# Kernel optimization log

Hardware: AMD Instinct MI355X
Metric: run time of the kernel (lower is better)

The kernel has to match this reference:

```python
import jax, jax.numpy as jnp
import numpy as np

B, T, C, HS = 512, 256, 384, 64

def setup_inputs() -> dict:
    key = jax.random.key(0)
    kx, kq, kk, kv = jax.random.split(key, 4)
    x = jax.random.normal(kx, (B, T, C), dtype=jnp.float32)
    Wq = jax.random.normal(kq, (C, HS), dtype=jnp.float32) * (C ** -0.5)
    Wk = jax.random.normal(kk, (C, HS), dtype=jnp.float32) * (C ** -0.5)
    Wv = jax.random.normal(kv, (C, HS), dtype=jnp.float32) * (C ** -0.5)
    return {"x": x, "Wq": Wq, "Wk": Wk, "Wv": Wv}

def reference(x, Wq, Wk, Wv):
    # single-head causal self-attention (dropout = identity in eval mode)
    q = jnp.einsum('btc,ch->bth', x, Wq)   # [B,T,HS]
    k = jnp.einsum('btc,ch->bth', x, Wk)   # [B,T,HS]
    v = jnp.einsum('btc,ch->bth', x, Wv)   # [B,T,HS]
    scale = k.shape[-1] ** -0.5
    wei = jnp.einsum('bqh,bkh->bqk', q, k) * scale  # [B,T,T]
    causal = jnp.tril(jnp.ones((T, T), dtype=bool))
    wei = jnp.where(causal, wei, -jnp.inf)
    wei = jax.nn.softmax(wei, axis=-1)
    out = jnp.einsum('bqk,bkh->bqh', wei, v)  # [B,T,HS]
    return out
```

## Files before the change

kernel.cpp:

```cpp
#include <hip/hip_runtime.h>


typedef float f32x4 __attribute__((ext_vector_type(4)));
typedef __bf16 bf16x8 __attribute__((ext_vector_type(8)));
typedef short s16x8 __attribute__((ext_vector_type(8)));

constexpr int T_ = 256;
constexpr int C_ = 384;
constexpr int HS_ = 64;
constexpr int QKVE = 512 * 256 * 64;

__device__ __forceinline__ short f2bs(float v) {
  __bf16 b = (__bf16)v;
  return __builtin_bit_cast(short, b);
}

__device__ __forceinline__ f32x4 mfma16(bf16x8 a, bf16x8 b, f32x4 c) {
  return __builtin_amdgcn_mfma_f32_16x16x32_bf16(a, b, c, 0, 0, 0);
}

__device__ __forceinline__ void gl_lds16(const short* g, short* l) {
  __builtin_amdgcn_global_load_lds((const __attribute__((address_space(1))) void*)g,
                                   (__attribute__((address_space(3))) void*)l,
                                   16, 0, 0);
}

__global__ void prep_wt_kernel(const float* __restrict__ Wq,
                               const float* __restrict__ Wk,
                               const float* __restrict__ Wv,
                               short* __restrict__ wt) {
  int idx = blockIdx.x * 256 + threadIdx.x;
  if (idx >= 192 * 384) return;
  int n = idx / 384;
  int k = idx - n * 384;
  const float* W = (n < 64) ? Wq : (n < 128) ? Wk : Wv;
  int h = n & 63;
  wt[idx] = f2bs(W[k * 64 + h]);
}

__global__ __launch_bounds__(256, 3) void qkv_proj(const float* __restrict__ x,
                                                   const short* __restrict__ wt,
                                                   short* __restrict__ ws) {
  __shared__ __align__(16) short wtile[2][4 * 192 * 8];
  __shared__ __align__(16) short vbuf[128][65];

  short* qg = ws;
  short* kg = ws + QKVE;
  short* vtg = ws + 2 * QKVE;

  const int blk = blockIdx.x;
  const int b = blk >> 1;
  const int rowbase = (blk & 1) * 128;
  const int tid = threadIdx.x;
  const int w = tid >> 6;
  const int lane = tid & 63;
  const int lr = tid & 15;
  const int lg = lane >> 4;

  const float* xb = x + (size_t)b * (T_ * C_);

  auto stage = [&](int buf, int ks) {
#pragma unroll
    for (int i = 0; i < 3; ++i) {
      int c = i * 256 + w * 64 + lane;
      int n = c % 192;
      int lgc = c / 192;
      const short* src = wt + n * 384 + ks * 32 + lgc * 8;
      short* dst = &wtile[buf][(i * 256 + w * 64) * 8];
      gl_lds16(src, dst);
    }
  };

  f32x4 xf[2][2], xn[2][2];
  auto loadx = [&](f32x4 dst[2][2], int ks) {
#pragma unroll
    for (int m = 0; m < 2; ++m) {
      int row = rowbase + (2 * w + m) * 16 + lr;
      const f32x4* p = reinterpret_cast<const f32x4*>(xb + (size_t)row * C_ + ks * 32 + lg * 8);
      dst[m][0] = p[0];
      dst[m][1] = p[1];
    }
  };

  f32x4 acc[2][12];
#pragma unroll
  for (int m = 0; m < 2; ++m)
#pragma unroll
    for (int nt = 0; nt < 12; ++nt) acc[m][nt] = f32x4{0.f, 0.f, 0.f, 0.f};

  stage(0, 0);
  loadx(xf, 0);
  __syncthreads();

  for (int ks = 0; ks < 12; ++ks) {
    const int cur = ks & 1;
    if (ks < 11) {
      stage(cur ^ 1, ks + 1);
      loadx(xn, ks + 1);
    }
    bf16x8 a[2];
#pragma unroll
    for (int m = 0; m < 2; ++m) {
      bf16x8 t;
      t[0] = (__bf16)xf[m][0][0]; t[1] = (__bf16)xf[m][0][1];
      t[2] = (__bf16)xf[m][0][2]; t[3] = (__bf16)xf[m][0][3];
      t[4] = (__bf16)xf[m][1][0]; t[5] = (__bf16)xf[m][1][1];
      t[6] = (__bf16)xf[m][1][2]; t[7] = (__bf16)xf[m][1][3];
      a[m] = t;
    }
#pragma unroll
    for (int nt = 0; nt < 12; ++nt) {
      bf16x8 bw = *reinterpret_cast<const bf16x8*>(&wtile[cur][(lg * 192 + nt * 16 + lr) * 8]);
      acc[0][nt] = mfma16(a[0], bw, acc[0][nt]);
      acc[1][nt] = mfma16(a[1], bw, acc[1][nt]);
    }
    __syncthreads();
    if (ks < 11) {
#pragma unroll
      for (int m = 0; m < 2; ++m) {
        xf[m][0] = xn[m][0];
        xf[m][1] = xn[m][1];
      }
    }
  }

  const float QSCALE = 0.125f * 1.44269504f;
#pragma unroll
  for (int nt = 0; nt < 12; ++nt) {
    const int which = nt >> 2;
    const int hb = (nt & 3) * 16 + lr;
#pragma unroll
    for (int m = 0; m < 2; ++m) {
#pragma unroll
      for (int j = 0; j < 4; ++j) {
        int t = rowbase + (2 * w + m) * 16 + lg * 4 + j;
        float v = acc[m][nt][j];
        if (which == 0) {
          qg[(size_t)b * 16384 + t * 64 + hb] = f2bs(v * QSCALE);
        } else if (which == 1) {
          kg[(size_t)b * 16384 + t * 64 + (hb ^ ((t & 7) << 3))] = f2bs(v);
        } else {
          vbuf[t - rowbase][hb] = f2bs(v);
        }
      }
    }
  }
  __syncthreads();

#pragma unroll
  for (int r = 0; r < 4; ++r) {
    int c = r * 256 + tid;
    int h = c >> 4;
    int i = c & 15;
    s16x8 tv;
#pragma unroll
    for (int j = 0; j < 8; ++j) tv[j] = vbuf[i * 8 + j][h];
    int tokbase = (rowbase + i * 8) ^ ((h & 7) << 3);
    *reinterpret_cast<s16x8*>(vtg + (size_t)b * 16384 + h * 256 + tokbase) = tv;
  }
}

__global__ __launch_bounds__(512, 4) void attn(const short* __restrict__ ws,
                                               float* __restrict__ out) {
  __shared__ __align__(16) short KS[256 * 64];
  __shared__ __align__(16) short VT[64 * 256];
  __shared__ __align__(16) short PB[8][16 * 40];

  const short* qg = ws;
  const short* kg = ws + QKVE;
  const short* vtg = ws + 2 * QKVE;

  const int b = blockIdx.x;
  const int tid = threadIdx.x;
  const int w = tid >> 6;
  const int lane = tid & 63;
  const int lr = tid & 15;
  const int lg = lane >> 4;

#pragma unroll
  for (int i = 0; i < 4; ++i) {
    int ch = w * 4 + i;
    gl_lds16(kg + (size_t)b * 16384 + ch * 512 + lane * 8, &KS[ch * 512]);
    gl_lds16(vtg + (size_t)b * 16384 + ch * 512 + lane * 8, &VT[ch * 512]);
  }
  __syncthreads();

  for (int pass = 0; pass < 2; ++pass) {
    const int t = pass ? (15 - w) : w;
    const short* qrow = qg + (size_t)b * 16384 + (t * 16 + lr) * 64;
    bf16x8 aq0 = *reinterpret_cast<const bf16x8*>(qrow + lg * 8);
    bf16x8 aq1 = *reinterpret_cast<const bf16x8*>(qrow + 32 + lg * 8);

    f32x4 o[4];
    float mrun[4], lrun[4];
#pragma unroll
    for (int nt = 0; nt < 4; ++nt) o[nt] = f32x4{0.f, 0.f, 0.f, 0.f};
#pragma unroll
    for (int j = 0; j < 4; ++j) { mrun[j] = -1e30f; lrun[j] = 0.f; }

    const int nkt = (t >> 1) + 1;
    for (int kt = 0; kt < nkt; ++kt) {
      f32x4 s0 = f32x4{0.f, 0.f, 0.f, 0.f};
      f32x4 s1 = f32x4{0.f, 0.f, 0.f, 0.f};
      {
        int kr0 = kt * 32 + lr;
        int kr1 = kr0 + 16;
        bf16x8 b00 = *reinterpret_cast<const bf16x8*>(&KS[kr0 * 64 + ((lg * 8) ^ ((kr0 & 7) << 3))]);
        bf16x8 b01 = *reinterpret_cast<const bf16x8*>(&KS[kr0 * 64 + ((32 + lg * 8) ^ ((kr0 & 7) << 3))]);
        bf16x8 b10 = *reinterpret_cast<const bf16x8*>(&KS[kr1 * 64 + ((lg * 8) ^ ((kr1 & 7) << 3))]);
        bf16x8 b11 = *reinterpret_cast<const bf16x8*>(&KS[kr1 * 64 + ((32 + lg * 8) ^ ((kr1 & 7) << 3))]);
        s0 = mfma16(aq0, b00, s0);
        s0 = mfma16(aq1, b01, s0);
        s1 = mfma16(aq0, b10, s1);
        s1 = mfma16(aq1, b11, s1);
      }

      if (kt == nkt - 1) {
#pragma unroll
        for (int j = 0; j < 4; ++j) {
          int row = t * 16 + lg * 4 + j;
          if (kt * 32 + lr > row)      s0[j] = -1e30f;
          if (kt * 32 + 16 + lr > row) s1[j] = -1e30f;
        }
      }

      float alpha[4];
#pragma unroll
      for (int j = 0; j < 4; ++j) {
        float mx = fmaxf(s0[j], s1[j]);
        mx = fmaxf(mx, __shfl_xor(mx, 1));
        mx = fmaxf(mx, __shfl_xor(mx, 2));
        mx = fmaxf(mx, __shfl_xor(mx, 4));
        mx = fmaxf(mx, __shfl_xor(mx, 8));
        float mnew = fmaxf(mrun[j], mx);
        float al = exp2f(mrun[j] - mnew);
        mrun[j] = mnew;
        alpha[j] = al;
        float e0 = exp2f(s0[j] - mnew);
        float e1 = exp2f(s1[j] - mnew);
        float rs = e0 + e1;
        rs += __shfl_xor(rs, 1);
        rs += __shfl_xor(rs, 2);
        rs += __shfl_xor(rs, 4);
        rs += __shfl_xor(rs, 8);
        lrun[j] = lrun[j] * al + rs;
        int prow = lg * 4 + j;
        PB[w][prow * 40 + lr] = f2bs(e0);
        PB[w][prow * 40 + 16 + lr] = f2bs(e1);
      }

#pragma unroll
      for (int nt = 0; nt < 4; ++nt) {
        o[nt][0] *= alpha[0];
        o[nt][1] *= alpha[1];
        o[nt][2] *= alpha[2];
        o[nt][3] *= alpha[3];
      }
      bf16x8 ap = *reinterpret_cast<const bf16x8*>(&PB[w][lr * 40 + lg * 8]);
#pragma unroll
      for (int nt = 0; nt < 4; ++nt) {
        int h = nt * 16 + lr;
        bf16x8 bv = *reinterpret_cast<const bf16x8*>(&VT[h * 256 + ((kt * 32 + lg * 8) ^ ((h & 7) << 3))]);
        o[nt] = mfma16(ap, bv, o[nt]);
      }
    }

    float inv[4];
#pragma unroll
    for (int j = 0; j < 4; ++j) inv[j] = 1.0f / lrun[j];
    float* ob = out + ((size_t)b * T_ + t * 16 + lg * 4) * HS_;
#pragma unroll
    for (int nt = 0; nt < 4; ++nt)
#pragma unroll
      for (int j = 0; j < 4; ++j)
        ob[j * HS_ + nt * 16 + lr] = o[nt][j] * inv[j];
  }
}

__device__ __forceinline__ int qswz(int row, int h) {
  return row * 64 + (h ^ ((row & 7) << 3));
}
__device__ __forceinline__ int vswz(int h, int tok) {
  return h * 256 + (tok ^ ((h & 7) << 3));
}

__global__ __launch_bounds__(512, 1) void fused_head(const float* __restrict__ x,
                                                     const short* __restrict__ wt,
                                                     float* __restrict__ out) {
  __shared__ __align__(16) short QS[256 * 64];
  __shared__ __align__(16) short KS[256 * 64];
  __shared__ __align__(16) short VT[64 * 256];
  __shared__ __align__(16) short PB[8][16 * 40];

  const int b = blockIdx.x;
  const int tid = threadIdx.x;
  const int w = tid >> 6;
  const int lr = tid & 15;
  const int lg = (tid & 63) >> 4;

  const float* xb = x + (size_t)b * (T_ * C_);

  f32x4 acc[2][12];
#pragma unroll
  for (int m = 0; m < 2; ++m)
#pragma unroll
    for (int nt = 0; nt < 12; ++nt) acc[m][nt] = f32x4{0.f, 0.f, 0.f, 0.f};

#pragma unroll
  for (int ks = 0; ks < 12; ++ks) {
    bf16x8 a[2];
#pragma unroll
    for (int m = 0; m < 2; ++m) {
      int row = (2 * w + m) * 16 + lr;
      const f32x4* p = reinterpret_cast<const f32x4*>(xb + row * C_ + ks * 32 + lg * 8);
      f32x4 f0 = p[0];
      f32x4 f1 = p[1];
      bf16x8 t;
      t[0] = (__bf16)f0[0]; t[1] = (__bf16)f0[1]; t[2] = (__bf16)f0[2]; t[3] = (__bf16)f0[3];
      t[4] = (__bf16)f1[0]; t[5] = (__bf16)f1[1]; t[6] = (__bf16)f1[2]; t[7] = (__bf16)f1[3];
      a[m] = t;
    }
#pragma unroll
    for (int nt = 0; nt < 12; ++nt) {
      bf16x8 bw = *reinterpret_cast<const bf16x8*>(wt + (nt * 16 + lr) * 384 + ks * 32 + lg * 8);
      acc[0][nt] = mfma16(a[0], bw, acc[0][nt]);
      acc[1][nt] = mfma16(a[1], bw, acc[1][nt]);
    }
  }

  const float QSCALE = 0.125f * 1.44269504f;
#pragma unroll
  for (int nt = 0; nt < 12; ++nt) {
    const int which = nt >> 2;
    const int hb = (nt & 3) * 16 + lr;
#pragma unroll
    for (int m = 0; m < 2; ++m) {
      const int rbase = (2 * w + m) * 16 + lg * 4;
#pragma unroll
      for (int j = 0; j < 4; ++j) {
        int row = rbase + j;
        float v = acc[m][nt][j];
        if (which == 0)      QS[qswz(row, hb)] = f2bs(v * QSCALE);
        else if (which == 1) KS[qswz(row, hb)] = f2bs(v);
        else                 VT[vswz(hb, row)] = f2bs(v);
      }
    }
  }

  __syncthreads();

  for (int pass = 0; pass < 2; ++pass) {
    const int t = pass ? (15 - w) : w;
    const int qrow = t * 16 + lr;
    bf16x8 aq0 = *reinterpret_cast<const bf16x8*>(&QS[qswz(qrow, lg * 8)]);
    bf16x8 aq1 = *reinterpret_cast<const bf16x8*>(&QS[qswz(qrow, 32 + lg * 8)]);

    f32x4 o[4];
    float mrun[4], lrun[4];
#pragma unroll
    for (int nt = 0; nt < 4; ++nt) o[nt] = f32x4{0.f, 0.f, 0.f, 0.f};
#pragma unroll
    for (int j = 0; j < 4; ++j) { mrun[j] = -1e30f; lrun[j] = 0.f; }

    const int nkt = (t >> 1) + 1;
    for (int kt = 0; kt < nkt; ++kt) {
      f32x4 s0 = f32x4{0.f, 0.f, 0.f, 0.f};
      f32x4 s1 = f32x4{0.f, 0.f, 0.f, 0.f};
      {
        int kr0 = kt * 32 + lr;
        int kr1 = kr0 + 16;
        bf16x8 b00 = *reinterpret_cast<const bf16x8*>(&KS[qswz(kr0, lg * 8)]);
        bf16x8 b01 = *reinterpret_cast<const bf16x8*>(&KS[qswz(kr0, 32 + lg * 8)]);
        bf16x8 b10 = *reinterpret_cast<const bf16x8*>(&KS[qswz(kr1, lg * 8)]);
        bf16x8 b11 = *reinterpret_cast<const bf16x8*>(&KS[qswz(kr1, 32 + lg * 8)]);
        s0 = mfma16(aq0, b00, s0);
        s0 = mfma16(aq1, b01, s0);
        s1 = mfma16(aq0, b10, s1);
        s1 = mfma16(aq1, b11, s1);
      }

      if (kt == nkt - 1) {
#pragma unroll
        for (int j = 0; j < 4; ++j) {
          int row = t * 16 + lg * 4 + j;
          if (kt * 32 + lr > row)      s0[j] = -1e30f;
          if (kt * 32 + 16 + lr > row) s1[j] = -1e30f;
        }
      }

      float alpha[4];
#pragma unroll
      for (int j = 0; j < 4; ++j) {
        float mx = fmaxf(s0[j], s1[j]);
        mx = fmaxf(mx, __shfl_xor(mx, 1));
        mx = fmaxf(mx, __shfl_xor(mx, 2));
        mx = fmaxf(mx, __shfl_xor(mx, 4));
        mx = fmaxf(mx, __shfl_xor(mx, 8));
        float mnew = fmaxf(mrun[j], mx);
        float al = exp2f(mrun[j] - mnew);
        mrun[j] = mnew;
        alpha[j] = al;
        float e0 = exp2f(s0[j] - mnew);
        float e1 = exp2f(s1[j] - mnew);
        float rs = e0 + e1;
        rs += __shfl_xor(rs, 1);
        rs += __shfl_xor(rs, 2);
        rs += __shfl_xor(rs, 4);
        rs += __shfl_xor(rs, 8);
        lrun[j] = lrun[j] * al + rs;
        int prow = lg * 4 + j;
        PB[w][prow * 40 + lr] = f2bs(e0);
        PB[w][prow * 40 + 16 + lr] = f2bs(e1);
      }

#pragma unroll
      for (int nt = 0; nt < 4; ++nt) {
        o[nt][0] *= alpha[0];
        o[nt][1] *= alpha[1];
        o[nt][2] *= alpha[2];
        o[nt][3] *= alpha[3];
      }
      bf16x8 ap = *reinterpret_cast<const bf16x8*>(&PB[w][lr * 40 + lg * 8]);
#pragma unroll
      for (int nt = 0; nt < 4; ++nt) {
        int h = nt * 16 + lr;
        bf16x8 bv = *reinterpret_cast<const bf16x8*>(&VT[vswz(h, kt * 32 + lg * 8)]);
        o[nt] = mfma16(ap, bv, o[nt]);
      }
    }

    float inv[4];
#pragma unroll
    for (int j = 0; j < 4; ++j) inv[j] = 1.0f / lrun[j];
    float* ob = out + ((size_t)b * T_ + t * 16 + lg * 4) * HS_;
#pragma unroll
    for (int nt = 0; nt < 4; ++nt)
#pragma unroll
      for (int j = 0; j < 4; ++j)
        ob[j * HS_ + nt * 16 + lr] = o[nt][j] * inv[j];
  }
}

extern "C" void kernel_launch(void* const* d_in, const int* in_sizes, int n_in,
                              void* d_out, int out_size, void* d_ws, size_t ws_size,
                              hipStream_t stream) {
  const float* x = (const float*)d_in[0];
  const float* Wq = (const float*)d_in[1];
  const float* Wk = (const float*)d_in[2];
  const float* Wv = (const float*)d_in[3];
  float* out = (float*)d_out;
  short* ws = (short*)d_ws;

  const size_t need = ((size_t)3 * QKVE + 192 * 384) * sizeof(short);

  if (ws_size >= need) {
    short* wt = ws + 3 * QKVE;
    prep_wt_kernel<<<288, 256, 0, stream>>>(Wq, Wk, Wv, wt);
    qkv_proj<<<1024, 256, 0, stream>>>(x, wt, ws);
    attn<<<512, 512, 0, stream>>>(ws, out);
  } else {
    short* wt = ws;
    prep_wt_kernel<<<288, 256, 0, stream>>>(Wq, Wk, Wv, wt);
    fused_head<<<512, 512, 0, stream>>>(x, wt, out);
  }
}
```

Before: 368.1 us.

## Keep full swizzled weight matrix resident in LDS for persistent QKV projection

The QKV projection kernel now loads the whole 192x384 bf16 weight matrix into LDS once per block, using an XOR-swizzled layout written by the prep kernel, so bank conflicts stay low. It then runs 256 blocks of 1024 threads, each wave handling two 16-row tiles with register double-buffered x loads and no per-k-step barriers. The V transpose through LDS is replaced with direct scattered global stores. This is meant to remove repeated weight staging and synchronisation, but it uses about 144KB of LDS per block, limiting occupancy to one block per CU, and the V writes become uncoalesced 2-byte stores.

```diff
diff --git a/kernel.cpp b/kernel.cpp
--- a/kernel.cpp
+++ b/kernel.cpp
@@ -32,131 +32,109 @@
   int idx = blockIdx.x * 256 + threadIdx.x;
   if (idx >= 192 * 384) return;
   int n = idx / 384;
-  int k = idx - n * 384;
+  int kpos = idx - n * 384;
+  int cpos = kpos >> 3;
+  int inner = kpos & 7;
+  int k = ((cpos ^ (n & 7)) << 3) | inner;
   const float* W = (n < 64) ? Wq : (n < 128) ? Wk : Wv;
   int h = n & 63;
   wt[idx] = f2bs(W[k * 64 + h]);
 }
 
-__global__ __launch_bounds__(256, 3) void qkv_proj(const float* __restrict__ x,
-                                                   const short* __restrict__ wt,
-                                                   short* __restrict__ ws) {
-  __shared__ __align__(16) short wtile[2][4 * 192 * 8];
-  __shared__ __align__(16) short vbuf[128][65];
+__global__ __launch_bounds__(1024, 4) void qkv_proj(const float* __restrict__ x,
+                                                    const short* __restrict__ wt,
+                                                    short* __restrict__ ws) {
+  __shared__ __align__(16) short WL[192 * 384];
 
   short* qg = ws;
   short* kg = ws + QKVE;
   short* vtg = ws + 2 * QKVE;
 
-  const int blk = blockIdx.x;
-  const int b = blk >> 1;
-  const int rowbase = (blk & 1) * 128;
   const int tid = threadIdx.x;
   const int w = tid >> 6;
-  const int lane = tid & 63;
   const int lr = tid & 15;
-  const int lg = lane >> 4;
-
-  const float* xb = x + (size_t)b * (T_ * C_);
-
-  auto stage = [&](int buf, int ks) {
-#pragma unroll
-    for (int i = 0; i < 3; ++i) {
-      int c = i * 256 + w * 64 + lane;
-      int n = c % 192;
-      int lgc = c / 192;
-      const short* src = wt + n * 384 + ks * 32 + lgc * 8;
-      short* dst = &wtile[buf][(i * 256 + w * 64) * 8];
-      gl_lds16(src, dst);
-    }
-  };
-
-  f32x4 xf[2][2], xn[2][2];
-  auto loadx = [&](f32x4 dst[2][2], int ks) {
-#pragma unroll
-    for (int m = 0; m < 2; ++m) {
-      int row = rowbase + (2 * w + m) * 16 + lr;
-      const f32x4* p = reinterpret_cast<const f32x4*>(xb + (size_t)row * C_ + ks * 32 + lg * 8);
-      dst[m][0] = p[0];
-      dst[m][1] = p[1];
-    }
-  };
-
-  f32x4 acc[2][12];
-#pragma unroll
-  for (int m = 0; m < 2; ++m)
-#pragma unroll
-    for (int nt = 0; nt < 12; ++nt) acc[m][nt] = f32x4{0.f, 0.f, 0.f, 0.f};
-
-  stage(0, 0);
-  loadx(xf, 0);
+  const int lg = (tid & 63) >> 4;
+
+#pragma unroll
+  for (int i = 0; i < 9; ++i) {
+    gl_lds16(wt + (i * 1024 + tid) * 8, &WL[(i * 1024 + w * 64) * 8]);
+  }
   __syncthreads();
 
-  for (int ks = 0; ks < 12; ++ks) {
-    const int cur = ks & 1;
-    if (ks < 11) {
-      stage(cur ^ 1, ks + 1);
-      loadx(xn, ks + 1);
-    }
-    bf16x8 a[2];
-#pragma unroll
-    for (int m = 0; m < 2; ++m) {
-      bf16x8 t;
-      t[0] = (__bf16)xf[m][0][0]; t[1] = (__bf16)xf[m][0][1];
-      t[2] = (__bf16)xf[m][0][2]; t[3] = (__bf16)xf[m][0][3];
-      t[4] = (__bf16)xf[m][1][0]; t[5] = (__bf16)xf[m][1][1];
-      t[6] = (__bf16)xf[m][1][2]; t[7] = (__bf16)xf[m][1][3];
-      a[m] = t;
-    }
+  const int tile0 = blockIdx.x * 16 + w;
+  const float* rp0 = x + ((size_t)tile0 * 16 + lr) * C_;
+  const float* rp1 = x + ((size_t)(tile0 + 4096) * 16 + lr) * C_;
+
+  f32x4 xa[2][2];
+  {
+    const f32x4* p = reinterpret_cast<const f32x4*>(rp0 + lg * 8);
+    xa[0][0] = p[0];
+    xa[0][1] = p[1];
+  }
+
+  const float QSCALE = 0.125f * 1.44269504f;
+
+  for (int t = 0; t < 2; ++t) {
+    const float* rpc = t ? rp1 : rp0;
+    f32x4 acc[12];
+#pragma unroll
+    for (int nt = 0; nt < 12; ++nt) acc[nt] = f32x4{0.f, 0.f, 0.f, 0.f};
+
+#pragma unroll
+    for (int ks = 0; ks < 12; ++ks) {
+      const int slot = ks & 1;
+      if (ks < 11) {
+        const f32x4* p = reinterpret_cast<const f32x4*>(rpc + (ks + 1) * 32 + lg * 8);
+        xa[slot ^ 1][0] = p[0];
+        xa[slot ^ 1][1] = p[1];
+      } else if (t == 0) {
+        const f32x4* p = reinterpret_cast<const f32x4*>(rp1 + lg * 8);
+        xa[0][0] = p[0];
+        xa[0][1] = p[1];
+      }
+
+      bf16x8 a;
+      a[0] = (__bf16)xa[slot][0][0]; a[1] = (__bf16)xa[slot][0][1];
+      a[2] = (__bf16)xa[slot][0][2]; a[3] = (__bf16)xa[slot][0][3];
+      a[4] = (__bf16)xa[slot][1][0]; a[5] = (__bf16)xa[slot][1][1];
+      a[6] = (__bf16)xa[slot][1][2]; a[7] = (__bf16)xa[slot][1][3];
+
+#pragma unroll
+      for (int hlf = 0; hlf < 2; ++hlf) {
+        bf16x8 bb[6];
+#pragma unroll
+        for (int i2 = 0; i2 < 6; ++i2) {
+          int nt = hlf * 6 + i2;
+          int n = nt * 16 + lr;
+          int cpos = (ks * 4 + lg) ^ (lr & 7);
+          bb[i2] = *reinterpret_cast<const bf16x8*>(&WL[n * 384 + cpos * 8]);
+        }
+#pragma unroll
+        for (int i2 = 0; i2 < 6; ++i2)
+          acc[hlf * 6 + i2] = mfma16(a, bb[i2], acc[hlf * 6 + i2]);
+      }
+    }
+
+    const int tg = t ? (tile0 + 4096) : tile0;
 #pragma unroll
     for (int nt = 0; nt < 12; ++nt) {
-      bf16x8 bw = *reinterpret_cast<const bf16x8*>(&wtile[cur][(lg * 192 + nt * 16 + lr) * 8]);
-      acc[0][nt] = mfma16(a[0], bw, acc[0][nt]);
-      acc[1][nt] = mfma16(a[1], bw, acc[1][nt]);
-    }
-    __syncthreads();
-    if (ks < 11) {
-#pragma unroll
-      for (int m = 0; m < 2; ++m) {
-        xf[m][0] = xn[m][0];
-        xf[m][1] = xn[m][1];
-      }
-    }
-  }
-
-  const float QSCALE = 0.125f * 1.44269504f;
-#pragma unroll
-  for (int nt = 0; nt < 12; ++nt) {
-    const int which = nt >> 2;
-    const int hb = (nt & 3) * 16 + lr;
-#pragma unroll
-    for (int m = 0; m < 2; ++m) {
+      const int which = nt >> 2;
+      const int hb = (nt & 3) * 16 + lr;
 #pragma unroll
       for (int j = 0; j < 4; ++j) {
-        int t = rowbase + (2 * w + m) * 16 + lg * 4 + j;
-        float v = acc[m][nt][j];
+        size_t grow = (size_t)tg * 16 + lg * 4 + j;
+        float v = acc[nt][j];
         if (which == 0) {
-          qg[(size_t)b * 16384 + t * 64 + hb] = f2bs(v * QSCALE);
+          qg[grow * 64 + hb] = f2bs(v * QSCALE);
         } else if (which == 1) {
-          kg[(size_t)b * 16384 + t * 64 + (hb ^ ((t & 7) << 3))] = f2bs(v);
+          kg[grow * 64 + (hb ^ (((int)grow & 7) << 3))] = f2bs(v);
         } else {
-          vbuf[t - rowbase][hb] = f2bs(v);
+          int h = (nt - 8) * 16 + lr;
+          int tokloc = (int)(grow & 255);
+          vtg[(grow >> 8) * 16384 + h * 256 + (tokloc ^ ((h & 7) << 3))] = f2bs(v);
         }
       }
     }
-  }
-  __syncthreads();
-
-#pragma unroll
-  for (int r = 0; r < 4; ++r) {
-    int c = r * 256 + tid;
-    int h = c >> 4;
-    int i = c & 15;
-    s16x8 tv;
-#pragma unroll
-    for (int j = 0; j < 8; ++j) tv[j] = vbuf[i * 8 + j][h];
-    int tokbase = (rowbase + i * 8) ^ ((h & 7) << 3);
-    *reinterpret_cast<s16x8*>(vtg + (size_t)b * 16384 + h * 256 + tokbase) = tv;
   }
 }
 
@@ -322,7 +300,9 @@
     }
 #pragma unroll
     for (int nt = 0; nt < 12; ++nt) {
-      bf16x8 bw = *reinterpret_cast<const bf16x8*>(wt + (nt * 16 + lr) * 384 + ks * 32 + lg * 8);
+      int n = nt * 16 + lr;
+      int cpos = (ks * 4 + lg) ^ (lr & 7);
+      bf16x8 bw = *reinterpret_cast<const bf16x8*>(wt + n * 384 + cpos * 8);
       acc[0][nt] = mfma16(a[0], bw, acc[0][nt]);
       acc[1][nt] = mfma16(a[1], bw, acc[1][nt]);
     }
@@ -456,7 +436,7 @@
   if (ws_size >= need) {
     short* wt = ws + 3 * QKVE;
     prep_wt_kernel<<<288, 256, 0, stream>>>(Wq, Wk, Wv, wt);
-    qkv_proj<<<1024, 256, 0, stream>>>(x, wt, ws);
+    qkv_proj<<<256, 1024, 0, stream>>>(x, wt, ws);
     attn<<<512, 512, 0, stream>>>(ws, out);
   } else {
     short* wt = ws;
```

New measurement: 762.2 us. 2.07x slower.
